# Performance work log

Measured on AMD Instinct MI355X. Metric: run time of the kernel, lower is better.

## Reference

```python
import jax, jax.numpy as jnp
import numpy as np
from math import sqrt, exp

EMBED_DIM = 1024
HEAD_DIM = 128
LAMBDA_INIT = 0.8 - 0.6 * exp(-0.3 * 0)  # layer_index = 0


def setup_inputs() -> dict:
    key = jax.random.key(0)
    ks = jax.random.split(key, 12)
    B, Tq, Tk = 4, 2048, 2048
    s = 1.0 / sqrt(EMBED_DIM)
    return {
        "x": jax.random.normal(ks[0], (B, Tq, EMBED_DIM), jnp.float32),
        "encoder_out": jax.random.normal(ks[1], (B, Tk, EMBED_DIM), jnp.float32),
        "W_q": jax.random.normal(ks[2], (EMBED_DIM, HEAD_DIM), jnp.float32) * s,
        "b_q": jnp.zeros((HEAD_DIM,), jnp.float32),
        "W_k": jax.random.normal(ks[3], (EMBED_DIM, HEAD_DIM), jnp.float32) * s,
        "b_k": jnp.zeros((HEAD_DIM,), jnp.float32),
        "W_v": jax.random.normal(ks[4], (EMBED_DIM, HEAD_DIM), jnp.float32) * s,
        "b_v": jnp.zeros((HEAD_DIM,), jnp.float32),
        "lambda_q1": jax.random.normal(ks[5], (HEAD_DIM,), jnp.float32) * 0.1,
        "lambda_k1": jax.random.normal(ks[6], (HEAD_DIM,), jnp.float32) * 0.1,
        "lambda_q2": jax.random.normal(ks[7], (HEAD_DIM,), jnp.float32) * 0.1,
        "lambda_k2": jax.random.normal(ks[8], (HEAD_DIM,), jnp.float32) * 0.1,
        "lambda_init": jnp.asarray(LAMBDA_INIT, jnp.float32),
    }


def reference(x, encoder_out, W_q, b_q, W_k, b_k, W_v, b_v,
              lambda_q1, lambda_k1, lambda_q2, lambda_k2, lambda_init):
    # scalar learned lambda
    lam = jnp.exp(lambda_q1 @ lambda_k1) - jnp.exp(lambda_q2 @ lambda_k2) + lambda_init
    q = x @ W_q + b_q                      # [B, Tq, D]
    k = encoder_out @ W_k + b_k            # [B, Tk, D]
    v = encoder_out @ W_v + b_v            # [B, Tk, D]
    d = HEAD_DIM // 2
    q1, q2 = q[..., :d], q[..., d:]
    k1, k2 = k[..., :d], k[..., d:]
    scale = 1.0 / sqrt(d)
    s1 = jnp.einsum("bqd,bkd->bqk", q1, k1) * scale
    s2 = jnp.einsum("bqd,bkd->bqk", q2, k2) * scale
    w = jax.nn.softmax(s1, axis=-1) - lam * jax.nn.softmax(s2, axis=-1)
    return jnp.einsum("bqk,bkd->bqd", w, v)   # [B, Tq, D]
```

## Files before the change

kernel.cpp:

```cpp
#include <hip/hip_runtime.h>
#include <hip/hip_bf16.h>


#define TQ 2048
#define TK 2048
#define EMB 1024
#define HD 128
#define MQ 8192

typedef __attribute__((ext_vector_type(8))) short short8;
typedef __attribute__((ext_vector_type(4))) float floatx4;

__device__ __forceinline__ unsigned short f2bf(float f) {
  union { float f; unsigned u; } v; v.f = f;
  unsigned r = v.u + 0x7fffu + ((v.u >> 16) & 1u);
  return (unsigned short)(r >> 16);
}
__device__ __forceinline__ float bf2f(unsigned short s) {
  union { unsigned u; float f; } v; v.u = ((unsigned)s) << 16;
  return v.f;
}

typedef const __attribute__((address_space(1))) unsigned int guint;
typedef __attribute__((address_space(3))) unsigned int luint;
__device__ __forceinline__ void gl16(const void* g, void* l) {
  __builtin_amdgcn_global_load_lds((guint*)g, (luint*)l, 16, 0, 0);
}

__global__ __launch_bounds__(256) void cvtWT_kernel(
    const float* __restrict__ Wq, const float* __restrict__ Wk,
    const float* __restrict__ Wv, unsigned short* __restrict__ WqT,
    unsigned short* __restrict__ WkT, unsigned short* __restrict__ WvT,
    const float* __restrict__ lq1, const float* __restrict__ lk1,
    const float* __restrict__ lq2, const float* __restrict__ lk2,
    const float* __restrict__ linit, float* __restrict__ lam_out) {
  const int g = blockIdx.y;
  if (g == 3) {
    if (blockIdx.x == 0 && threadIdx.x < 64) {
      int j = threadIdx.x;
      float s1 = lq1[j] * lk1[j] + lq1[j + 64] * lk1[j + 64];
      float s2 = lq2[j] * lk2[j] + lq2[j + 64] * lk2[j + 64];
      for (int off = 1; off < 64; off <<= 1) {
        s1 += __shfl_xor(s1, off);
        s2 += __shfl_xor(s2, off);
      }
      if (j == 0) lam_out[0] = __expf(s1) - __expf(s2) + linit[0];
    }
    return;
  }
  const float* W = (g == 0) ? Wq : (g == 1) ? Wk : Wv;
  unsigned short* WT = (g == 0) ? WqT : (g == 1) ? WkT : WvT;
  int idx = blockIdx.x * 256 + threadIdx.x;
  int n = idx >> 10, k = idx & 1023;
  WT[idx] = f2bf(W[(size_t)k * HD + n]);
}

__global__ __launch_bounds__(256) void gemm_proj_kernel(
    const float* __restrict__ x, const float* __restrict__ enc,
    const unsigned short* __restrict__ WqT, const unsigned short* __restrict__ WkT,
    const unsigned short* __restrict__ WvT,
    const float* __restrict__ bq, const float* __restrict__ bk,
    const float* __restrict__ bv,
    unsigned short* __restrict__ qb, unsigned short* __restrict__ kb,
    unsigned short* __restrict__ vbT) {
  __shared__ __align__(16) float Ab[2][32 * 64];
  __shared__ __align__(16) unsigned short Bb[2][128 * 64];
  const int t = threadIdx.x;
  const int w = t >> 6, lane = t & 63;
  const int lo = lane & 15, quad = lane >> 4;
  const int wm = w & 1, wn = w >> 1;
  const int g = blockIdx.y;
  const size_t m0 = (size_t)blockIdx.x * 32;
  const float* A = (g == 0) ? x : enc;
  const unsigned short* BT = (g == 0) ? WqT : (g == 1) ? WkT : WvT;
  const float* bias = (g == 0) ? bq : (g == 1) ? bk : bv;

  const float* gA[2];
  int ldsAoff[2];
#pragma unroll
  for (int j = 0; j < 2; ++j) {
    int c = 2 * w + j;
    int row = 4 * c + (lane >> 4);
    int colb = ((lane & 15) * 16) ^ ((row & 7) << 4);
    gA[j] = A + (m0 + row) * EMB + (colb >> 2);
    ldsAoff[j] = c * 1024;
  }
  const unsigned short* gB[4];
  int ldsBoff[4];
#pragma unroll
  for (int j = 0; j < 4; ++j) {
    int c = 4 * w + j;
    int row = 8 * c + (lane >> 3);
    int colb = ((lane & 7) * 16) ^ ((row & 7) << 4);
    gB[j] = BT + (size_t)row * EMB + (colb >> 1);
    ldsBoff[j] = c * 1024;
  }

  floatx4 acc[4];
  const floatx4 zz = {0.f, 0.f, 0.f, 0.f};
#pragma unroll
  for (int i = 0; i < 4; ++i) acc[i] = zz;

  const int xr = (lo & 7) << 4;

  auto stage = [&](int kt, int bsel) {
#pragma unroll
    for (int j = 0; j < 2; ++j) gl16(gA[j] + kt, (char*)&Ab[bsel][0] + ldsAoff[j]);
#pragma unroll
    for (int j = 0; j < 4; ++j) gl16(gB[j] + kt, (char*)&Bb[bsel][0] + ldsBoff[j]);
  };

  auto compute = [&](int bsel) {
    const char* Arow = (const char*)&Ab[bsel][(16 * wm + lo) * 64];
    const char* Bbase = (const char*)&Bb[bsel][0];
#pragma unroll
    for (int ks = 0; ks < 2; ++ks) {
      int a0 = (ks * 128 + quad * 32) ^ xr;
      float4 fa = *(const float4*)(Arow + a0);
      float4 fb = *(const float4*)(Arow + (a0 ^ 16));
      short8 af;
      af[0] = (short)f2bf(fa.x); af[1] = (short)f2bf(fa.y);
      af[2] = (short)f2bf(fa.z); af[3] = (short)f2bf(fa.w);
      af[4] = (short)f2bf(fb.x); af[5] = (short)f2bf(fb.y);
      af[6] = (short)f2bf(fb.z); af[7] = (short)f2bf(fb.w);
      int b0 = (ks * 64 + quad * 16) ^ xr;
#pragma unroll
      for (int nt = 0; nt < 4; ++nt) {
        int row = wn * 64 + nt * 16 + lo;
        short8 bfr = *(const short8*)(Bbase + row * 128 + b0);
        acc[nt] = __builtin_amdgcn_mfma_f32_16x16x32_bf16(af, bfr, acc[nt], 0, 0, 0);
      }
    }
  };

  stage(0, 0);
  __syncthreads();

  for (int kt = 0; kt < EMB; kt += 128) {
    stage(kt + 64, 1);
    compute(0);
    __syncthreads();
    if (kt + 128 < EMB) stage(kt + 128, 0);
    compute(1);
    __syncthreads();
  }

  const int mrow = 16 * wm + quad * 4;
  if (g < 2) {
    unsigned short* Y = (g == 0) ? qb : kb;
    const float sc = (g == 0) ? 0.125f : 1.0f;
#pragma unroll
    for (int nt = 0; nt < 4; ++nt) {
      float bn = bias[wn * 64 + nt * 16 + lo];
#pragma unroll
      for (int r = 0; r < 4; ++r)
        Y[(m0 + mrow + r) * HD + wn * 64 + nt * 16 + lo] = f2bf((acc[nt][r] + bn) * sc);
    }
  } else {
#pragma unroll
    for (int nt = 0; nt < 4; ++nt) {
      float bn = bias[wn * 64 + nt * 16 + lo];
      unsigned long long pk = 0;
#pragma unroll
      for (int r = 0; r < 4; ++r)
        pk |= (unsigned long long)f2bf(acc[nt][r] + bn) << (16 * r);
      *(unsigned long long*)&vbT[(size_t)(wn * 64 + nt * 16 + lo) * MQ + m0 + mrow] = pk;
    }
  }
}

__global__ __launch_bounds__(512, 4) void attn_split_kernel(
    const unsigned short* __restrict__ qb, const unsigned short* __restrict__ kb,
    const unsigned short* __restrict__ vbT,
    unsigned short* __restrict__ pO1, unsigned short* __restrict__ pO2,
    float2* __restrict__ pstats, int nkeys) {
  __shared__ __align__(16) unsigned short Kls[64][136];
  __shared__ __align__(16) unsigned short Vt[128][72];
  __shared__ __align__(16) unsigned short Pls[8][16][72];

  const int t = threadIdx.x;
  const int w = t >> 6;
  const int g = w >> 2;
  const int wv = w & 3;
  const int lane = t & 63;
  const int lo = lane & 15;
  const int quad = lane >> 4;
  const int q8 = quad * 8;
  const int b = blockIdx.y;
  const int q0 = blockIdx.x * 64;
  const int ksp = blockIdx.z;
  const int kt0 = ksp * nkeys;
  const int ksTot = TK / nkeys;
  const size_t kbase = (size_t)b * TK;

  const size_t qrow = (size_t)b * TQ + q0 + wv * 16 + lo;
  short8 qf[2];
#pragma unroll
  for (int ks = 0; ks < 2; ++ks)
    qf[ks] = *(const short8*)&qb[qrow * HD + g * 64 + ks * 32 + q8];

  floatx4 o[8];
  const floatx4 zz = {0.f, 0.f, 0.f, 0.f};
#pragma unroll
  for (int i = 0; i < 8; ++i) o[i] = zz;
  float m[4], l[4];
#pragma unroll
  for (int r = 0; r < 4; ++r) { m[r] = -1e30f; l[r] = 0.f; }

  for (int kt = kt0; kt < kt0 + nkeys; kt += 64) {
#pragma unroll
    for (int i = 0; i < 2; ++i) {
      int c = t + 512 * i;
      int key = c >> 4, f0 = (c & 15) * 8;
      *(int4*)&Kls[key][f0] =
          *(const int4*)&kb[(kbase + kt + key) * HD + f0];
      int f = c >> 3, k0 = (c & 7) * 8;
      *(int4*)&Vt[f][k0] =
          *(const int4*)&vbT[(size_t)f * MQ + kbase + kt + k0];
    }
    __syncthreads();

    floatx4 s[4];
#pragma unroll
    for (int i = 0; i < 4; ++i) s[i] = zz;
#pragma unroll
    for (int ks = 0; ks < 2; ++ks)
#pragma unroll
      for (int nt = 0; nt < 4; ++nt) {
        short8 kf = *(const short8*)&Kls[nt * 16 + lo][g * 64 + ks * 32 + q8];
        s[nt] = __builtin_amdgcn_mfma_f32_16x16x32_bf16(qf[ks], kf, s[nt], 0, 0, 0);
      }

    float tm[4];
#pragma unroll
    for (int r = 0; r < 4; ++r) {
      float a = fmaxf(fmaxf(s[0][r], s[1][r]), fmaxf(s[2][r], s[3][r]));
#pragma unroll
      for (int oo = 1; oo < 16; oo <<= 1) a = fmaxf(a, __shfl_xor(a, oo));
      tm[r] = a;
    }
    bool grow = false;
#pragma unroll
    for (int r = 0; r < 4; ++r) grow = grow || (tm[r] > m[r] + 5.f);
    if (__any(grow)) {
#pragma unroll
      for (int r = 0; r < 4; ++r) {
        float mn = fmaxf(m[r], tm[r]);
        float al = __expf(m[r] - mn);
        m[r] = mn;
        l[r] *= al;
#pragma unroll
        for (int nt = 0; nt < 8; ++nt) o[nt][r] *= al;
      }
    }
#pragma unroll
    for (int r = 0; r < 4; ++r) {
      float ls = 0.f;
#pragma unroll
      for (int nt = 0; nt < 4; ++nt) {
        float p = __expf(s[nt][r] - m[r]);
        ls += p;
        Pls[w][quad * 4 + r][nt * 16 + lo] = f2bf(p);
      }
#pragma unroll
      for (int oo = 1; oo < 16; oo <<= 1) ls += __shfl_xor(ls, oo);
      l[r] += ls;
    }

#pragma unroll
    for (int ks = 0; ks < 2; ++ks) {
      short8 p8 = *(const short8*)&Pls[w][lo][ks * 32 + q8];
#pragma unroll
      for (int nt = 0; nt < 8; ++nt) {
        short8 vf = *(const short8*)&Vt[nt * 16 + lo][ks * 32 + q8];
        o[nt] = __builtin_amdgcn_mfma_f32_16x16x32_bf16(p8, vf, o[nt], 0, 0, 0);
      }
    }
    __syncthreads();
  }

  unsigned short* Y = g ? pO2 : pO1;
#pragma unroll
  for (int r = 0; r < 4; ++r) {
    int rowb = q0 + wv * 16 + quad * 4 + r;
    size_t idx = ((size_t)(ksp * 4 + b)) * TQ + rowb;
    if (lo == 0)
      pstats[((size_t)(g * ksTot + ksp) * 4 + b) * TQ + rowb] = make_float2(m[r], l[r]);
#pragma unroll
    for (int nt = 0; nt < 8; ++nt)
      Y[idx * HD + nt * 16 + lo] = f2bf(o[nt][r]);
  }
}

__global__ __launch_bounds__(256) void attn_combine_kernel(
    const unsigned short* __restrict__ pO1, const unsigned short* __restrict__ pO2,
    const float2* __restrict__ pstats, const float* __restrict__ lam_ptr,
    float* __restrict__ out, int ksn) {
  const int t = threadIdx.x;
  const int b = blockIdx.y;
  const int row = blockIdx.x * 16 + (t >> 4);
  const int dg = t & 15;

  float m1s[8], l1s[8], m2s[8], l2s[8];
  float M1 = -1e30f, M2 = -1e30f;
  for (int s = 0; s < ksn; ++s) {
    float2 fa = pstats[((size_t)(s) * 4 + b) * TQ + row];
    float2 fb = pstats[((size_t)(ksn + s) * 4 + b) * TQ + row];
    m1s[s] = fa.x; l1s[s] = fa.y; m2s[s] = fb.x; l2s[s] = fb.y;
    M1 = fmaxf(M1, fa.x); M2 = fmaxf(M2, fb.x);
  }
  float L1 = 0.f, L2 = 0.f, e1[8], e2[8];
  for (int s = 0; s < ksn; ++s) {
    e1[s] = __expf(m1s[s] - M1); e2[s] = __expf(m2s[s] - M2);
    L1 += l1s[s] * e1[s]; L2 += l2s[s] * e2[s];
  }
  float a1[8], a2[8];
#pragma unroll
  for (int j = 0; j < 8; ++j) { a1[j] = 0.f; a2[j] = 0.f; }
  for (int s = 0; s < ksn; ++s) {
    size_t base = (((size_t)(s * 4 + b)) * TQ + row) * HD + dg * 8;
    int4 r1 = *(const int4*)&pO1[base];
    int4 r2 = *(const int4*)&pO2[base];
    const unsigned short* u1 = (const unsigned short*)&r1;
    const unsigned short* u2 = (const unsigned short*)&r2;
#pragma unroll
    for (int j = 0; j < 8; ++j) {
      a1[j] += bf2f(u1[j]) * e1[s];
      a2[j] += bf2f(u2[j]) * e2[s];
    }
  }
  const float i1 = 1.f / L1;
  const float i2 = lam_ptr[0] / L2;
  float4* op = (float4*)&out[((size_t)b * TQ + row) * HD + dg * 8];
  op[0] = make_float4(a1[0] * i1 - a2[0] * i2, a1[1] * i1 - a2[1] * i2,
                      a1[2] * i1 - a2[2] * i2, a1[3] * i1 - a2[3] * i2);
  op[1] = make_float4(a1[4] * i1 - a2[4] * i2, a1[5] * i1 - a2[5] * i2,
                      a1[6] * i1 - a2[6] * i2, a1[7] * i1 - a2[7] * i2);
}

__global__ __launch_bounds__(256) void attn_check_kernel(
    const unsigned short* __restrict__ qb, const unsigned short* __restrict__ kb,
    const unsigned short* __restrict__ vbT, const float* __restrict__ lamp,
    float* __restrict__ out) {
  __shared__ float qsh[HD];
  __shared__ float sred[4][4];
  const int t = threadIdx.x;
  const int w = t >> 6, lane = t & 63;
  const int bb = blockIdx.x & 3;
  const int q = (int)((blockIdx.x * 997u + 13u) & 2047u);
  const int dc = (int)((blockIdx.x * 37u + 5u) & 127u);

  const unsigned short* qr = &qb[((size_t)bb * TQ + q) * HD];
  if (t < HD) qsh[t] = bf2f(qr[t]);
  __syncthreads();

  float mx1 = -1e30f, mx2 = -1e30f;
  for (int it = 0; it < 8; ++it) {
    int key = t + 256 * it;
    const unsigned* kr = (const unsigned*)&kb[((size_t)bb * TK + key) * HD];
    float s1 = 0.f, s2 = 0.f;
#pragma unroll 8
    for (int du = 0; du < 32; ++du) {
      unsigned u1 = kr[du], u2 = kr[32 + du];
      s1 += qsh[2 * du] * bf2f((unsigned short)u1) +
            qsh[2 * du + 1] * bf2f((unsigned short)(u1 >> 16));
      s2 += qsh[64 + 2 * du] * bf2f((unsigned short)u2) +
            qsh[64 + 2 * du + 1] * bf2f((unsigned short)(u2 >> 16));
    }
    mx1 = fmaxf(mx1, s1); mx2 = fmaxf(mx2, s2);
  }
  for (int o = 1; o < 64; o <<= 1) {
    mx1 = fmaxf(mx1, __shfl_xor(mx1, o));
    mx2 = fmaxf(mx2, __shfl_xor(mx2, o));
  }
  if (lane == 0) { sred[0][w] = mx1; sred[1][w] = mx2; }
  __syncthreads();
  mx1 = fmaxf(fmaxf(sred[0][0], sred[0][1]), fmaxf(sred[0][2], sred[0][3]));
  mx2 = fmaxf(fmaxf(sred[1][0], sred[1][1]), fmaxf(sred[1][2], sred[1][3]));
  __syncthreads();

  float l1 = 0.f, l2 = 0.f, o1 = 0.f, o2 = 0.f;
  for (int it = 0; it < 8; ++it) {
    int key = t + 256 * it;
    const unsigned* kr = (const unsigned*)&kb[((size_t)bb * TK + key) * HD];
    float s1 = 0.f, s2 = 0.f;
#pragma unroll 8
    for (int du = 0; du < 32; ++du) {
      unsigned u1 = kr[du], u2 = kr[32 + du];
      s1 += qsh[2 * du] * bf2f((unsigned short)u1) +
            qsh[2 * du + 1] * bf2f((unsigned short)(u1 >> 16));
      s2 += qsh[64 + 2 * du] * bf2f((unsigned short)u2) +
            qsh[64 + 2 * du + 1] * bf2f((unsigned short)(u2 >> 16));
    }
    float p1 = __expf(s1 - mx1), p2 = __expf(s2 - mx2);
    float v = bf2f(vbT[(size_t)dc * MQ + bb * TK + key]);
    l1 += p1; l2 += p2; o1 += p1 * v; o2 += p2 * v;
  }
  for (int o = 1; o < 64; o <<= 1) {
    l1 += __shfl_xor(l1, o); l2 += __shfl_xor(l2, o);
    o1 += __shfl_xor(o1, o); o2 += __shfl_xor(o2, o);
  }
  if (lane == 0) { sred[0][w] = l1; sred[1][w] = l2; sred[2][w] = o1; sred[3][w] = o2; }
  __syncthreads();
  if (t == 0) {
    l1 = sred[0][0] + sred[0][1] + sred[0][2] + sred[0][3];
    l2 = sred[1][0] + sred[1][1] + sred[1][2] + sred[1][3];
    o1 = sred[2][0] + sred[2][1] + sred[2][2] + sred[2][3];
    o2 = sred[3][0] + sred[3][1] + sred[3][2] + sred[3][3];
    float res = o1 / l1 - lamp[0] * (o2 / l2);
    float got = out[((size_t)bb * TQ + q) * HD + dc];
    if (!(fabsf(res - got) <= 0.02f)) out[0] = 1.0e7f;
  }
}

extern "C" void kernel_launch(void* const* d_in, const int* in_sizes, int n_in,
                              void* d_out, int out_size, void* d_ws, size_t ws_size,
                              hipStream_t stream) {
  const float* x    = (const float*)d_in[0];
  const float* enc  = (const float*)d_in[1];
  const float* Wq   = (const float*)d_in[2];
  const float* bq   = (const float*)d_in[3];
  const float* Wk   = (const float*)d_in[4];
  const float* bk   = (const float*)d_in[5];
  const float* Wv   = (const float*)d_in[6];
  const float* bv   = (const float*)d_in[7];
  const float* lq1  = (const float*)d_in[8];
  const float* lk1  = (const float*)d_in[9];
  const float* lq2  = (const float*)d_in[10];
  const float* lk2  = (const float*)d_in[11];
  const float* lini = (const float*)d_in[12];
  float* out = (float*)d_out;

  char* p = (char*)d_ws;
  float* lam = (float*)p;                       p += 256;
  unsigned short* qb  = (unsigned short*)p;     p += (size_t)MQ * HD * 2;
  unsigned short* kb  = (unsigned short*)p;     p += (size_t)MQ * HD * 2;
  unsigned short* vbT = (unsigned short*)p;     p += (size_t)MQ * HD * 2;
  unsigned short* WqT = (unsigned short*)p;     p += (size_t)EMB * HD * 2;
  unsigned short* WkT = (unsigned short*)p;     p += (size_t)EMB * HD * 2;
  unsigned short* WvT = (unsigned short*)p;     p += (size_t)EMB * HD * 2;
  const size_t base_need = (size_t)(p - (char*)d_ws);

  const size_t per_ks = (size_t)4 * TQ * 16 + 2ull * 4 * TQ * HD * 2;
  int KS = 4;
  while (KS > 1 && base_need + (size_t)KS * per_ks > ws_size) KS >>= 1;

  float2* pstats = (float2*)p;                  p += (size_t)KS * 4 * TQ * 16;
  unsigned short* pO1 = (unsigned short*)p;     p += (size_t)KS * 4 * TQ * HD * 2;
  unsigned short* pO2 = (unsigned short*)p;

  hipLaunchKernelGGL(cvtWT_kernel, dim3(512, 4), dim3(256), 0, stream,
                     Wq, Wk, Wv, WqT, WkT, WvT, lq1, lk1, lq2, lk2, lini, lam);
  hipLaunchKernelGGL(gemm_proj_kernel, dim3(MQ / 32, 3), dim3(256), 0, stream,
                     x, enc, WqT, WkT, WvT, bq, bk, bv, qb, kb, vbT);
  hipLaunchKernelGGL(attn_split_kernel, dim3(TQ / 64, 4, KS), dim3(512), 0, stream,
                     qb, kb, vbT, pO1, pO2, pstats, TK / KS);
  hipLaunchKernelGGL(attn_combine_kernel, dim3(TQ / 16, 4), dim3(256), 0, stream,
                     pO1, pO2, pstats, lam, out, KS);
  hipLaunchKernelGGL(attn_check_kernel, dim3(128), dim3(256), 0, stream,
                     qb, kb, vbT, lam, out);
}
```

Measured before the change: 209.0 us.

## Double-buffer K/V tiles with direct global-to-LDS loads and XOR-swizzled layout

The attention split kernel now keeps two LDS buffers for the K and V tiles and fills them with direct global-to-LDS copies (gl16), so the next tile loads while the current one is computed. The padded layouts are replaced by XOR-swizzled unpadded ones to avoid bank conflicts, and the P scratch reuses the K buffer after a barrier to save LDS. Occupancy is pinned with waves_per_eu(4,4). The loop now steps 128 keys at a time, so it assumes nkeys is a multiple of 128 and depends on the barrier placement being correct when the K buffer is reused for P.

```diff
diff --git a/kernel.cpp b/kernel.cpp
--- a/kernel.cpp
+++ b/kernel.cpp
@@ -169,14 +169,14 @@
   }
 }
 
-__global__ __launch_bounds__(512, 4) void attn_split_kernel(
+__global__ __launch_bounds__(512)
+__attribute__((amdgpu_waves_per_eu(4, 4))) void attn_split_kernel(
     const unsigned short* __restrict__ qb, const unsigned short* __restrict__ kb,
     const unsigned short* __restrict__ vbT,
     unsigned short* __restrict__ pO1, unsigned short* __restrict__ pO2,
     float2* __restrict__ pstats, int nkeys) {
-  __shared__ __align__(16) unsigned short Kls[64][136];
-  __shared__ __align__(16) unsigned short Vt[128][72];
-  __shared__ __align__(16) unsigned short Pls[8][16][72];
+  __shared__ __align__(16) unsigned short KB[2][64 * 128];
+  __shared__ __align__(16) unsigned short VB[2][128 * 64];
 
   const int t = threadIdx.x;
   const int w = t >> 6;
@@ -186,6 +186,7 @@
   const int lo = lane & 15;
   const int quad = lane >> 4;
   const int q8 = quad * 8;
+  const int xr = (lo & 7) << 4;
   const int b = blockIdx.y;
   const int q0 = blockIdx.x * 64;
   const int ksp = blockIdx.z;
@@ -199,6 +200,21 @@
   for (int ks = 0; ks < 2; ++ks)
     qf[ks] = *(const short8*)&qb[qrow * HD + g * 64 + ks * 32 + q8];
 
+  const char* kSrc[2];
+  const char* vSrc[2];
+  int ldsOff[2];
+#pragma unroll
+  for (int j = 0; j < 2; ++j) {
+    int c = w + 8 * j;
+    int krow = c * 4 + (lane >> 4);
+    int kcolb = ((lane & 15) * 16) ^ ((krow & 7) << 4);
+    kSrc[j] = (const char*)&kb[(kbase + krow) * HD] + kcolb;
+    int f = c * 8 + (lane >> 3);
+    int vcolb = ((lane & 7) * 16) ^ ((f & 7) << 4);
+    vSrc[j] = (const char*)&vbT[(size_t)f * MQ + kbase] + vcolb;
+    ldsOff[j] = c * 1024;
+  }
+
   floatx4 o[8];
   const floatx4 zz = {0.f, 0.f, 0.f, 0.f};
 #pragma unroll
@@ -207,29 +223,32 @@
 #pragma unroll
   for (int r = 0; r < 4; ++r) { m[r] = -1e30f; l[r] = 0.f; }
 
-  for (int kt = kt0; kt < kt0 + nkeys; kt += 64) {
-#pragma unroll
-    for (int i = 0; i < 2; ++i) {
-      int c = t + 512 * i;
-      int key = c >> 4, f0 = (c & 15) * 8;
-      *(int4*)&Kls[key][f0] =
-          *(const int4*)&kb[(kbase + kt + key) * HD + f0];
-      int f = c >> 3, k0 = (c & 7) * 8;
-      *(int4*)&Vt[f][k0] =
-          *(const int4*)&vbT[(size_t)f * MQ + kbase + kt + k0];
-    }
+  auto stage = [&](int kt, int bsel) {
+#pragma unroll
+    for (int j = 0; j < 2; ++j) {
+      gl16(kSrc[j] + (size_t)kt * 256, (char*)&KB[bsel][0] + ldsOff[j]);
+      gl16(vSrc[j] + (size_t)kt * 2, (char*)&VB[bsel][0] + ldsOff[j]);
+    }
+  };
+
+  auto computeTile = [&](int bsel) {
+    const char* Kb = (const char*)&KB[bsel][0];
+    const char* Vb = (const char*)&VB[bsel][0];
+    char* Pb = (char*)&KB[bsel][0] + w * 2048;
+
+    floatx4 s[4];
+#pragma unroll
+    for (int i = 0; i < 4; ++i) s[i] = zz;
+#pragma unroll
+    for (int ks = 0; ks < 2; ++ks)
+#pragma unroll
+      for (int nt = 0; nt < 4; ++nt) {
+        int row = nt * 16 + lo;
+        int cb = (g * 128 + ks * 64 + quad * 16) ^ xr;
+        short8 kf = *(const short8*)(Kb + row * 256 + cb);
+        s[nt] = __builtin_amdgcn_mfma_f32_16x16x32_bf16(qf[ks], kf, s[nt], 0, 0, 0);
+      }
     __syncthreads();
-
-    floatx4 s[4];
-#pragma unroll
-    for (int i = 0; i < 4; ++i) s[i] = zz;
-#pragma unroll
-    for (int ks = 0; ks < 2; ++ks)
-#pragma unroll
-      for (int nt = 0; nt < 4; ++nt) {
-        short8 kf = *(const short8*)&Kls[nt * 16 + lo][g * 64 + ks * 32 + q8];
-        s[nt] = __builtin_amdgcn_mfma_f32_16x16x32_bf16(qf[ks], kf, s[nt], 0, 0, 0);
-      }
 
     float tm[4];
 #pragma unroll
@@ -256,11 +275,14 @@
 #pragma unroll
     for (int r = 0; r < 4; ++r) {
       float ls = 0.f;
+      int rr = quad * 4 + r;
+      int srr = (rr & 7) << 4;
 #pragma unroll
       for (int nt = 0; nt < 4; ++nt) {
         float p = __expf(s[nt][r] - m[r]);
         ls += p;
-        Pls[w][quad * 4 + r][nt * 16 + lo] = f2bf(p);
+        int pb = rr * 128 + (((nt * 16 + lo) * 2) ^ srr);
+        *(unsigned short*)(Pb + pb) = f2bf(p);
       }
 #pragma unroll
       for (int oo = 1; oo < 16; oo <<= 1) ls += __shfl_xor(ls, oo);
@@ -269,14 +291,25 @@
 
 #pragma unroll
     for (int ks = 0; ks < 2; ++ks) {
-      short8 p8 = *(const short8*)&Pls[w][lo][ks * 32 + q8];
+      int cb = (ks * 64 + quad * 16) ^ xr;
+      short8 p8 = *(const short8*)(Pb + lo * 128 + cb);
 #pragma unroll
       for (int nt = 0; nt < 8; ++nt) {
-        short8 vf = *(const short8*)&Vt[nt * 16 + lo][ks * 32 + q8];
+        short8 vf = *(const short8*)(Vb + (nt * 16 + lo) * 128 + cb);
         o[nt] = __builtin_amdgcn_mfma_f32_16x16x32_bf16(p8, vf, o[nt], 0, 0, 0);
       }
     }
     __syncthreads();
+  };
+
+  stage(kt0, 0);
+  __syncthreads();
+
+  for (int kt = kt0; kt < kt0 + nkeys; kt += 128) {
+    stage(kt + 64, 1);
+    computeTile(0);
+    if (kt + 128 < kt0 + nkeys) stage(kt + 128, 0);
+    computeTile(1);
   }
 
   unsigned short* Y = g ? pO2 : pO1;
```

Measured after the change: 215.5 us. 1.03x slower.
